# Kernel optimization log

Measured on AMD Instinct MI355X. Metric: run time of the kernel, lower is better.

The kernel has to match this reference:

```python
import jax, jax.numpy as jnp
import numpy as np

B, TQ, TK, DQ, DK, DV = 16, 1024, 1024, 1024, 1024, 1024


def setup_inputs() -> dict:
    key = jax.random.key(0)
    k1, k2, k3, k4, k5 = jax.random.split(key, 5)
    query = jax.random.normal(k1, (B, TQ, DQ), dtype=jnp.float32)
    keys = jax.random.normal(k2, (B, TK, DK), dtype=jnp.float32)
    values = jax.random.normal(k3, (B, TK, DV), dtype=jnp.float32)
    W = jax.random.normal(k4, (DQ, DK), dtype=jnp.float32) / np.sqrt(DQ)
    mask = jax.random.normal(k5, (B, TK), dtype=jnp.float32)
    return {"query": query, "keys": keys, "values": values, "W": W, "mask": mask}


def reference(query, keys, values, W, mask):
    # Bilinear (Luong 'general') score: weight[b,q,k] = query[b,q,:] @ W @ keys[b,k,:]
    qW = jnp.einsum('bqd,de->bqe', query, W)              # [B, Tq, Dk]
    weight = jnp.einsum('bqe,bke->bqk', qW, keys)         # [B, Tq, Tk]
    weight = weight + mask[:, None, :]                    # additive mask, broadcast over Tq
    score = jax.nn.softmax(weight, axis=-1)               # [B, Tq, Tk]
    ctx = jnp.einsum('bqk,bkv->bqv', score, values)       # [B, Tq, Dv]
    return (score, ctx)
```

## Files before the change

### kernel.cpp

```cpp
#include <hip/hip_runtime.h>
#include <hip/hip_bf16.h>

typedef _Float16 f16;
typedef __attribute__((ext_vector_type(8))) _Float16 half8;
typedef __attribute__((ext_vector_type(4))) float f32x4;

#define BM 128
#define BN 128
#define BK 32

__device__ __forceinline__ void gl2lds16(const f16* g, const f16* l) {
    __builtin_amdgcn_global_load_lds(
        (const __attribute__((address_space(1))) unsigned int*)g,
        (__attribute__((address_space(3))) unsigned int*)l, 16, 0, 0);
}

__global__ __launch_bounds__(256)
void cast_f16(const float* __restrict__ in, f16* __restrict__ out, long long n) {
    long long i = ((long long)blockIdx.x * 256 + threadIdx.x) * 8;
    if (i >= n) return;
    float4 a = *(const float4*)&in[i];
    float4 b = *(const float4*)&in[i + 4];
    union { f16 h[8]; uint4 q; } H;
    H.h[0] = (f16)a.x; H.h[1] = (f16)a.y; H.h[2] = (f16)a.z; H.h[3] = (f16)a.w;
    H.h[4] = (f16)b.x; H.h[5] = (f16)b.y; H.h[6] = (f16)b.z; H.h[7] = (f16)b.w;
    *(uint4*)&out[i] = H.q;
}

__global__ __launch_bounds__(256)
void transpose_f16(const float* __restrict__ in, f16* __restrict__ out,
                   int R, int C, long long in_stride, long long out_stride) {
    const int b = blockIdx.z;
    in += (size_t)b * in_stride;
    out += (size_t)b * out_stride;

    __shared__ float tile[32][33];
    const int r0 = blockIdx.y * 32, c0 = blockIdx.x * 32;
    const int t = threadIdx.x;
    const int tr = t >> 5, tc = t & 31;
    for (int i = 0; i < 4; i++)
        tile[tr + i * 8][tc] = in[(size_t)(r0 + tr + i * 8) * C + c0 + tc];
    __syncthreads();
    for (int i = 0; i < 4; i++) {
        float v = tile[tc][tr + i * 8];
        out[(size_t)(c0 + tr + i * 8) * R + r0 + tc] = (f16)v;
    }
}

template<int EPI>
__global__ __launch_bounds__(256)
void gemm_f16(const f16* __restrict__ A_, const f16* __restrict__ B_,
              float* __restrict__ Cf, f16* __restrict__ Ch,
              const float* __restrict__ mask,
              int M, int N, int K,
              long long batchA, long long batchB, long long batchC) {
    const int b = blockIdx.z;
    const int m0 = blockIdx.y * BM;
    const int n0 = blockIdx.x * BN;
    const int t = threadIdx.x;
    const int lane = t & 63, wv = t >> 6;
    const int wm = (wv >> 1) * 64, wn = (wv & 1) * 64;

    const f16* A = A_ + (size_t)b * batchA;
    const f16* B = B_ + (size_t)b * batchB;

    __shared__ alignas(16) f16 sA[BM][BK];
    __shared__ alignas(16) f16 sB[BN][BK];

    f32x4 acc[4][4];
    for (int mi = 0; mi < 4; mi++)
        for (int ni = 0; ni < 4; ni++)
            for (int r = 0; r < 4; r++) acc[mi][ni][r] = 0.0f;

    const int lrow = lane >> 2;
    const int lcol = (lane & 3) * 8;

    for (int k0 = 0; k0 < K; k0 += BK) {
#pragma unroll
        for (int i = 0; i < 2; i++) {
            const int r0 = (wv + 4 * i) * 16;
            gl2lds16(&A[(size_t)(m0 + r0 + lrow) * K + k0 + lcol], &sA[r0][0]);
            gl2lds16(&B[(size_t)(n0 + r0 + lrow) * K + k0 + lcol], &sB[r0][0]);
        }
        __syncthreads();

        const int fr = lane & 15, fq = (lane >> 4) * 8;
        half8 af[4], bf[4];
#pragma unroll
        for (int i = 0; i < 4; i++) {
            af[i] = *(const half8*)&sA[wm + i * 16 + fr][fq];
            bf[i] = *(const half8*)&sB[wn + i * 16 + fr][fq];
        }
#pragma unroll
        for (int mi = 0; mi < 4; mi++)
#pragma unroll
            for (int ni = 0; ni < 4; ni++)
                acc[mi][ni] = __builtin_amdgcn_mfma_f32_16x16x32_f16(af[mi], bf[ni], acc[mi][ni], 0, 0, 0);
        __syncthreads();
    }

    const int fr = lane & 15, q4 = (lane >> 4) * 4;
    for (int mi = 0; mi < 4; mi++)
        for (int ni = 0; ni < 4; ni++) {
            const int col = n0 + wn + ni * 16 + fr;
            float mv = 0.0f;
            if constexpr (EPI == 1) mv = mask[(size_t)b * N + col];
            for (int r = 0; r < 4; r++) {
                const int row = m0 + wm + mi * 16 + q4 + r;
                float v = acc[mi][ni][r];
                const size_t idx = (size_t)b * batchC + (size_t)row * N + col;
                if constexpr (EPI == 0) {
                    Cf[idx] = v;
                } else if constexpr (EPI == 1) {
                    Cf[idx] = v + mv;
                } else {
                    Ch[idx] = (f16)v;
                }
            }
        }
}

__global__ __launch_bounds__(256)
void softmax_rows(float* __restrict__ w, f16* __restrict__ sb) {
    const size_t row = blockIdx.x;
    float* p = w + row * 1024;
    const int t = threadIdx.x;
    const int wv = t >> 6, ln = t & 63;

    float4 v = *(const float4*)&p[t * 4];
    float m = fmaxf(fmaxf(v.x, v.y), fmaxf(v.z, v.w));
    for (int o = 32; o > 0; o >>= 1) m = fmaxf(m, __shfl_down(m, o));
    __shared__ float redm[4];
    if (ln == 0) redm[wv] = m;
    __syncthreads();
    m = fmaxf(fmaxf(redm[0], redm[1]), fmaxf(redm[2], redm[3]));

    float e0 = __expf(v.x - m), e1 = __expf(v.y - m);
    float e2 = __expf(v.z - m), e3 = __expf(v.w - m);
    float s = e0 + e1 + e2 + e3;
    for (int o = 32; o > 0; o >>= 1) s += __shfl_down(s, o);
    __shared__ float reds[4];
    if (ln == 0) reds[wv] = s;
    __syncthreads();
    s = reds[0] + reds[1] + reds[2] + reds[3];
    const float inv = 1.0f / s;

    float4 o4; o4.x = e0 * inv; o4.y = e1 * inv; o4.z = e2 * inv; o4.w = e3 * inv;
    *(float4*)&p[t * 4] = o4;
    union { f16 h[4]; uint2 q; } H;
    H.h[0] = (f16)o4.x; H.h[1] = (f16)o4.y; H.h[2] = (f16)o4.z; H.h[3] = (f16)o4.w;
    *(uint2*)&sb[row * 1024 + t * 4] = H.q;
}

extern "C" void kernel_launch(void* const* d_in, const int* in_sizes, int n_in,
                              void* d_out, int out_size, void* d_ws, size_t ws_size,
                              hipStream_t stream) {
    const int B = 16, T = 1024, D = 1024;
    const long long MAT = (long long)T * D;
    const long long BT = (long long)B * MAT;

    const float* query  = (const float*)d_in[0];
    const float* keys   = (const float*)d_in[1];
    const float* values = (const float*)d_in[2];
    const float* W      = (const float*)d_in[3];
    const float* mask   = (const float*)d_in[4];

    float* out = (float*)d_out;
    float* score_f = out;
    float* ctx_f   = out + (size_t)BT;

    char* ws = (char*)d_ws;
    f16* R1  = (f16*)ws;                   ws += (size_t)BT * 2;
    f16* R2  = (f16*)ws;                   ws += (size_t)BT * 2;
    f16* qw  = (f16*)ws;                   ws += (size_t)BT * 2;
    f16* wt  = (f16*)ws;                   ws += (size_t)MAT * 2;

    f16* qf = R1, *vt = R1;
    f16* kf = R2, *sc = R2;

    dim3 blk(256);

    cast_f16<<<dim3((unsigned)(BT / 2048)), blk, 0, stream>>>(query, qf, BT);
    transpose_f16<<<dim3(32, 32, 1), blk, 0, stream>>>(W, wt, D, D, 0, 0);

    gemm_f16<2><<<dim3(8, 128, 1), blk, 0, stream>>>(
        qf, wt, nullptr, qw, nullptr, B * T, D, D, 0, 0, 0);

    cast_f16<<<dim3((unsigned)(BT / 2048)), blk, 0, stream>>>(keys, kf, BT);

    gemm_f16<1><<<dim3(8, 8, B), blk, 0, stream>>>(
        qw, kf, score_f, nullptr, mask, T, T, D, MAT, MAT, MAT);

    transpose_f16<<<dim3(32, 32, B), blk, 0, stream>>>(values, vt, T, D, MAT, MAT);

    softmax_rows<<<B * T, blk, 0, stream>>>(score_f, sc);

    gemm_f16<0><<<dim3(8, 8, B), blk, 0, stream>>>(
        sc, vt, ctx_f, nullptr, nullptr, T, D, T, MAT, MAT, MAT);
}
```

Baseline: 488.6 us.

## Rewrite GEMM as 256x256 double-buffered, XOR-swizzled, 8-wave pipelined kernel

Replaces the 128x128x32 single-buffered GEMM with a 256x256x64 tile kernel using 512 threads, double-buffered LDS, XOR-swizzled LDS layout, and global-to-LDS loads for the next tile interleaved between four MFMA phases, with setprio hints and manual waitcnt barriers. The aim is to hide global load latency, reduce LDS bank conflicts and raise per-block arithmetic intensity. It uses far more registers (32 accumulators per wave) and 128KB of LDS, which may limit occupancy. Grids shrink to 256 blocks for the batched GEMMs, which may underfill the 256 CUs.

After: 426.5 us. 1.15x faster.

```diff
diff --git a/kernel.cpp b/kernel.cpp
--- a/kernel.cpp
+++ b/kernel.cpp
@@ -5,15 +5,17 @@
 typedef __attribute__((ext_vector_type(8))) _Float16 half8;
 typedef __attribute__((ext_vector_type(4))) float f32x4;
 
-#define BM 128
-#define BN 128
-#define BK 32
+#define BM 256
+#define BN 256
+#define BK 64
 
 __device__ __forceinline__ void gl2lds16(const f16* g, const f16* l) {
     __builtin_amdgcn_global_load_lds(
         (const __attribute__((address_space(1))) unsigned int*)g,
         (__attribute__((address_space(3))) unsigned int*)l, 16, 0, 0);
 }
+
+#define MFMA(d, a, b) d = __builtin_amdgcn_mfma_f32_16x16x32_f16(a, b, d, 0, 0, 0)
 
 __global__ __launch_bounds__(256)
 void cast_f16(const float* __restrict__ in, f16* __restrict__ out, long long n) {
@@ -48,71 +50,169 @@
 }
 
 template<int EPI>
-__global__ __launch_bounds__(256)
-void gemm_f16(const f16* __restrict__ A_, const f16* __restrict__ B_,
-              float* __restrict__ Cf, f16* __restrict__ Ch,
-              const float* __restrict__ mask,
-              int M, int N, int K,
-              long long batchA, long long batchB, long long batchC) {
+__global__ __launch_bounds__(512, 2)
+void gemm256(const f16* __restrict__ A_, const f16* __restrict__ B_,
+             float* __restrict__ Cf, f16* __restrict__ Ch,
+             const float* __restrict__ mask,
+             int M, int N, int K,
+             long long batchA, long long batchB, long long batchC) {
     const int b = blockIdx.z;
     const int m0 = blockIdx.y * BM;
     const int n0 = blockIdx.x * BN;
     const int t = threadIdx.x;
     const int lane = t & 63, wv = t >> 6;
-    const int wm = (wv >> 1) * 64, wn = (wv & 1) * 64;
+    const int wr = wv >> 2;
+    const int wc = wv & 3;
 
     const f16* A = A_ + (size_t)b * batchA;
     const f16* B = B_ + (size_t)b * batchB;
 
-    __shared__ alignas(16) f16 sA[BM][BK];
-    __shared__ alignas(16) f16 sB[BN][BK];
-
-    f32x4 acc[4][4];
-    for (int mi = 0; mi < 4; mi++)
+    __shared__ alignas(16) f16 sA[2][2][128][64];
+    __shared__ alignas(16) f16 sB[2][2][128][64];
+
+    const int srow  = wv * 16 + (lane >> 3);
+    const int gslot = (lane & 7) ^ (lane >> 3);
+
+    const f16* gAl  = A + (size_t)(m0 + srow) * K + gslot * 8;
+    const f16* gAl8 = gAl + (size_t)8 * K;
+    const f16* gAh  = gAl + (size_t)128 * K;
+    const f16* gAh8 = gAl8 + (size_t)128 * K;
+    const f16* gBl  = B + (size_t)(n0 + srow) * K + gslot * 8;
+    const f16* gBl8 = gBl + (size_t)8 * K;
+    const f16* gBh  = gBl + (size_t)128 * K;
+    const f16* gBh8 = gBl8 + (size_t)128 * K;
+
+    f32x4 acc[8][4];
+#pragma unroll
+    for (int i = 0; i < 8; i++)
+#pragma unroll
+        for (int j = 0; j < 4; j++)
+#pragma unroll
+            for (int r = 0; r < 4; r++) acc[i][j][r] = 0.0f;
+
+    gl2lds16(gAl,  &sA[0][0][wv * 16][0]); gl2lds16(gAl8, &sA[0][0][wv * 16 + 8][0]);
+    gl2lds16(gAh,  &sA[0][1][wv * 16][0]); gl2lds16(gAh8, &sA[0][1][wv * 16 + 8][0]);
+    gl2lds16(gBl,  &sB[0][0][wv * 16][0]); gl2lds16(gBl8, &sB[0][0][wv * 16 + 8][0]);
+    gl2lds16(gBh,  &sB[0][1][wv * 16][0]); gl2lds16(gBh8, &sB[0][1][wv * 16 + 8][0]);
+
+    const int fr  = lane & 15;
+    const int fq4 = lane >> 4;
+    const int NT  = K / BK;
+
+    half8 af[4][2], bA[2][2], bB[2][2];
+
+    for (int tt = 0; tt < NT; ++tt) {
+        const int c = tt & 1, cn = c ^ 1;
+        const size_t kg = (size_t)(tt + 1) * BK;
+        const bool nx = (tt + 1 < NT);
+
+        const f16* pa = &sA[c][wr][fr][0];
+        const f16* pb = &sB[c][wc >> 1][(wc & 1) * 64 + fr][0];
+        const int cs0 = ((0 + fq4) ^ (fr & 7)) * 8;
+        const int cs1 = ((4 + fq4) ^ (fr & 7)) * 8;
+
+        if (nx) {
+            gl2lds16(gAl + kg,  &sA[cn][0][wv * 16][0]);
+            gl2lds16(gAl8 + kg, &sA[cn][0][wv * 16 + 8][0]);
+            asm volatile("s_waitcnt vmcnt(2)\n\ts_barrier" ::: "memory");
+        } else {
+            asm volatile("s_waitcnt vmcnt(0)\n\ts_barrier" ::: "memory");
+        }
+#pragma unroll
+        for (int mi = 0; mi < 4; mi++) {
+            af[mi][0] = *(const half8*)(pa + mi * 1024 + cs0);
+            af[mi][1] = *(const half8*)(pa + mi * 1024 + cs1);
+        }
+#pragma unroll
+        for (int ni = 0; ni < 2; ni++) {
+            bA[ni][0] = *(const half8*)(pb + ni * 1024 + cs0);
+            bA[ni][1] = *(const half8*)(pb + ni * 1024 + cs1);
+        }
+        __builtin_amdgcn_s_setprio(1);
+#pragma unroll
+        for (int mi = 0; mi < 4; mi++)
+#pragma unroll
+            for (int ni = 0; ni < 2; ni++) {
+                MFMA(acc[mi][ni], af[mi][0], bA[ni][0]);
+                MFMA(acc[mi][ni], af[mi][1], bA[ni][1]);
+            }
+        __builtin_amdgcn_s_setprio(0);
+
+        if (nx) {
+            gl2lds16(gAh + kg,  &sA[cn][1][wv * 16][0]);
+            gl2lds16(gAh8 + kg, &sA[cn][1][wv * 16 + 8][0]);
+        }
+#pragma unroll
+        for (int ni = 0; ni < 2; ni++) {
+            bB[ni][0] = *(const half8*)(pb + (2 + ni) * 1024 + cs0);
+            bB[ni][1] = *(const half8*)(pb + (2 + ni) * 1024 + cs1);
+        }
+        __builtin_amdgcn_s_setprio(1);
+#pragma unroll
+        for (int mi = 0; mi < 4; mi++)
+#pragma unroll
+            for (int ni = 0; ni < 2; ni++) {
+                MFMA(acc[mi][2 + ni], af[mi][0], bB[ni][0]);
+                MFMA(acc[mi][2 + ni], af[mi][1], bB[ni][1]);
+            }
+        __builtin_amdgcn_s_setprio(0);
+
+        if (nx) {
+            gl2lds16(gBl + kg,  &sB[cn][0][wv * 16][0]);
+            gl2lds16(gBl8 + kg, &sB[cn][0][wv * 16 + 8][0]);
+        }
+#pragma unroll
+        for (int mi = 0; mi < 4; mi++) {
+            af[mi][0] = *(const half8*)(pa + (64 + mi * 16) * 64 + cs0);
+            af[mi][1] = *(const half8*)(pa + (64 + mi * 16) * 64 + cs1);
+        }
+        __builtin_amdgcn_s_setprio(1);
+#pragma unroll
+        for (int mi = 0; mi < 4; mi++)
+#pragma unroll
+            for (int ni = 0; ni < 2; ni++) {
+                MFMA(acc[4 + mi][2 + ni], af[mi][0], bB[ni][0]);
+                MFMA(acc[4 + mi][2 + ni], af[mi][1], bB[ni][1]);
+            }
+        __builtin_amdgcn_s_setprio(0);
+
+        if (nx) {
+            gl2lds16(gBh + kg,  &sB[cn][1][wv * 16][0]);
+            gl2lds16(gBh8 + kg, &sB[cn][1][wv * 16 + 8][0]);
+        }
+        __builtin_amdgcn_s_setprio(1);
+#pragma unroll
+        for (int mi = 0; mi < 4; mi++)
+#pragma unroll
+            for (int ni = 0; ni < 2; ni++) {
+                MFMA(acc[4 + mi][ni], af[mi][0], bA[ni][0]);
+                MFMA(acc[4 + mi][ni], af[mi][1], bA[ni][1]);
+            }
+        __builtin_amdgcn_s_setprio(0);
+        asm volatile("s_barrier" ::: "memory");
+    }
+
+    const int q4 = (lane >> 4) * 4;
+    float mv[4] = {0.f, 0.f, 0.f, 0.f};
+    if constexpr (EPI == 1) {
+#pragma unroll
         for (int ni = 0; ni < 4; ni++)
-            for (int r = 0; r < 4; r++) acc[mi][ni][r] = 0.0f;
-
-    const int lrow = lane >> 2;
-    const int lcol = (lane & 3) * 8;
-
-    for (int k0 = 0; k0 < K; k0 += BK) {
-#pragma unroll
-        for (int i = 0; i < 2; i++) {
-            const int r0 = (wv + 4 * i) * 16;
-            gl2lds16(&A[(size_t)(m0 + r0 + lrow) * K + k0 + lcol], &sA[r0][0]);
-            gl2lds16(&B[(size_t)(n0 + r0 + lrow) * K + k0 + lcol], &sB[r0][0]);
-        }
-        __syncthreads();
-
-        const int fr = lane & 15, fq = (lane >> 4) * 8;
-        half8 af[4], bf[4];
-#pragma unroll
-        for (int i = 0; i < 4; i++) {
-            af[i] = *(const half8*)&sA[wm + i * 16 + fr][fq];
-            bf[i] = *(const half8*)&sB[wn + i * 16 + fr][fq];
-        }
-#pragma unroll
-        for (int mi = 0; mi < 4; mi++)
-#pragma unroll
-            for (int ni = 0; ni < 4; ni++)
-                acc[mi][ni] = __builtin_amdgcn_mfma_f32_16x16x32_f16(af[mi], bf[ni], acc[mi][ni], 0, 0, 0);
-        __syncthreads();
+            mv[ni] = mask[(size_t)b * N + n0 + wc * 64 + ni * 16 + fr];
     }
-
-    const int fr = lane & 15, q4 = (lane >> 4) * 4;
-    for (int mi = 0; mi < 4; mi++)
+#pragma unroll
+    for (int mi = 0; mi < 8; mi++)
+#pragma unroll
         for (int ni = 0; ni < 4; ni++) {
-            const int col = n0 + wn + ni * 16 + fr;
-            float mv = 0.0f;
-            if constexpr (EPI == 1) mv = mask[(size_t)b * N + col];
+            const int col = n0 + wc * 64 + ni * 16 + fr;
+#pragma unroll
             for (int r = 0; r < 4; r++) {
-                const int row = m0 + wm + mi * 16 + q4 + r;
+                const int row = m0 + wr * 128 + mi * 16 + q4 + r;
+                const size_t idx = (size_t)b * batchC + (size_t)row * N + col;
                 float v = acc[mi][ni][r];
-                const size_t idx = (size_t)b * batchC + (size_t)row * N + col;
                 if constexpr (EPI == 0) {
                     Cf[idx] = v;
                 } else if constexpr (EPI == 1) {
-                    Cf[idx] = v + mv;
+                    Cf[idx] = v + mv[ni];
                 } else {
                     Ch[idx] = (f16)v;
                 }
@@ -179,22 +279,23 @@
     f16* kf = R2, *sc = R2;
 
     dim3 blk(256);
+    dim3 blk5(512);
 
     cast_f16<<<dim3((unsigned)(BT / 2048)), blk, 0, stream>>>(query, qf, BT);
     transpose_f16<<<dim3(32, 32, 1), blk, 0, stream>>>(W, wt, D, D, 0, 0);
 
-    gemm_f16<2><<<dim3(8, 128, 1), blk, 0, stream>>>(
+    gemm256<2><<<dim3(4, 64, 1), blk5, 0, stream>>>(
         qf, wt, nullptr, qw, nullptr, B * T, D, D, 0, 0, 0);
 
     cast_f16<<<dim3((unsigned)(BT / 2048)), blk, 0, stream>>>(keys, kf, BT);
 
-    gemm_f16<1><<<dim3(8, 8, B), blk, 0, stream>>>(
+    gemm256<1><<<dim3(4, 4, B), blk5, 0, stream>>>(
         qw, kf, score_f, nullptr, mask, T, T, D, MAT, MAT, MAT);
 
     transpose_f16<<<dim3(32, 32, B), blk, 0, stream>>>(values, vt, T, D, MAT, MAT);
 
     softmax_rows<<<B * T, blk, 0, stream>>>(score_f, sc);
 
-    gemm_f16<0><<<dim3(8, 8, B), blk, 0, stream>>>(
+    gemm256<0><<<dim3(4, 4, B), blk5, 0, stream>>>(
         sc, vt, ctx_f, nullptr, nullptr, T, D, T, MAT, MAT, MAT);
 }
```
